# Optimization experiments

Hardware: AMD Instinct MI355X
Metric: run time of the kernel (lower is better)

The kernel has to match this reference:

```python
import jax, jax.numpy as jnp
import numpy as np


def setup_inputs() -> dict:
    key = jax.random.key(0)
    k1, k2 = jax.random.split(key)
    B, C, H, W, S = 8, 128, 256, 256, 1024
    inp = jax.random.normal(k1, (B, C, H, W), dtype=jnp.float32)
    seg = jax.random.randint(k2, (B, H, W), 0, S, dtype=jnp.int32)
    return {"input": inp, "segLabels": seg, "num_segments": S}


def reference(input, segLabels, num_segments):
    # input: [B, C, H, W] float; segLabels: [B, H, W] int in [0, S)
    B, C, H, W = input.shape
    S = num_segments
    N = H * W
    # [B, N, C] pixel features
    feats = jnp.transpose(input.reshape(B, C, N), (0, 2, 1))
    # offset labels so each image's segments occupy a disjoint id range
    ids = (segLabels.reshape(B, N) + jnp.arange(B, dtype=segLabels.dtype)[:, None] * S).reshape(-1)
    flat = feats.reshape(B * N, C)
    sums = jax.ops.segment_sum(flat, ids, num_segments=B * S)          # [B*S, C]
    counts = jax.ops.segment_sum(jnp.ones((B * N,), dtype=input.dtype), ids, num_segments=B * S)  # [B*S]
    avg = sums / jnp.maximum(counts, 1.0)[:, None]
    return avg.reshape(B, S, C)
```

## Files before the change

kernel.cpp:

```cpp
#include <hip/hip_runtime.h>


#define BB 8
#define CC 128
#define NPIX 65536
#define SS 1024
#define TILE 4096
#define NTILES (NPIX / TILE)
#define THREADS 1024

#define POS_ELEMS (BB * NPIX)
#define OFF_ELEMS (BB * NTILES * SS)

__device__ __forceinline__ void lds_barrier() {
  asm volatile("s_waitcnt lgkmcnt(0)\n\ts_barrier" ::: "memory");
}

__global__ __launch_bounds__(THREADS, 1) void sort_kernel(
    const int* __restrict__ seg, unsigned short* __restrict__ pos,
    unsigned short* __restrict__ tileoff) {
  __shared__ unsigned int hist[SS];
  __shared__ unsigned int wsum[16];
  const int b   = blockIdx.x / NTILES;
  const int t   = blockIdx.x % NTILES;
  const int tid = threadIdx.x;

  hist[tid] = 0u;
  __syncthreads();

  const int base = b * NPIX + t * TILE;
  const int4 lab = reinterpret_cast<const int4*>(seg + base)[tid];
  const unsigned int r0 = atomicAdd(&hist[lab.x], 1u);
  const unsigned int r1 = atomicAdd(&hist[lab.y], 1u);
  const unsigned int r2 = atomicAdd(&hist[lab.z], 1u);
  const unsigned int r3 = atomicAdd(&hist[lab.w], 1u);
  __syncthreads();

  const unsigned int cnt = hist[tid];
  unsigned int v = cnt;
  #pragma unroll
  for (int off = 1; off < 64; off <<= 1) {
    const unsigned int u = __shfl_up(v, off);
    if ((tid & 63) >= off) v += u;
  }
  const int w = tid >> 6;
  if ((tid & 63) == 63) wsum[w] = v;
  __syncthreads();
  if (tid < 16) {
    unsigned int x = wsum[tid];
    #pragma unroll
    for (int off = 1; off < 16; off <<= 1) {
      const unsigned int u = __shfl_up(x, off);
      if (tid >= off) x += u;
    }
    wsum[tid] = x;
  }
  __syncthreads();
  const unsigned int woff = (w == 0) ? 0u : wsum[w - 1];
  const unsigned int excl = woff + v - cnt;
  tileoff[(b * NTILES + t) * SS + tid] = (unsigned short)excl;
  hist[tid] = excl;
  __syncthreads();

  ushort4 p4;
  p4.x = (unsigned short)(hist[lab.x] + r0);
  p4.y = (unsigned short)(hist[lab.y] + r1);
  p4.z = (unsigned short)(hist[lab.z] + r2);
  p4.w = (unsigned short)(hist[lab.w] + r3);
  reinterpret_cast<ushort4*>(pos + base)[tid] = p4;
}

__global__ __launch_bounds__(THREADS, 1) void aggr_kernel(
    const float* __restrict__ inp, const unsigned short* __restrict__ pos,
    const unsigned short* __restrict__ tileoff, float* __restrict__ out) {
  __shared__ float4 buf[TILE];
  __shared__ unsigned short offl[SS + 2];

  const int b   = blockIdx.x >> 5;
  const int c0  = (blockIdx.x & 31) << 2;
  const int tid = threadIdx.x;

  const float4* __restrict__ pl0 =
      reinterpret_cast<const float4*>(inp + ((size_t)b * CC + c0) * NPIX);
  const ushort4* __restrict__ pos4 =
      reinterpret_cast<const ushort4*>(pos + (size_t)b * NPIX);
  const int Q = NPIX / 4;

  float a0 = 0.f, a1 = 0.f, a2 = 0.f, a3 = 0.f;
  int cnt = 0;

  float4 cv0 = pl0[tid], cv1 = pl0[tid + Q];
  float4 cv2 = pl0[tid + 2 * Q], cv3 = pl0[tid + 3 * Q];
  ushort4 cp4 = pos4[tid];
  unsigned short coff = tileoff[(b * NTILES + 0) * SS + tid];

  for (int t = 0; t < NTILES; ++t) {
    lds_barrier();
    if (tid == 0) offl[SS] = (unsigned short)TILE;
    offl[tid] = coff;
    buf[cp4.x] = make_float4(cv0.x, cv1.x, cv2.x, cv3.x);
    buf[cp4.y] = make_float4(cv0.y, cv1.y, cv2.y, cv3.y);
    buf[cp4.z] = make_float4(cv0.z, cv1.z, cv2.z, cv3.z);
    buf[cp4.w] = make_float4(cv0.w, cv1.w, cv2.w, cv3.w);

    const int tn = (t + 1 < NTILES) ? t + 1 : t;
    const int pn = tn * (TILE / 4) + tid;
    const float4 nv0 = pl0[pn], nv1 = pl0[pn + Q];
    const float4 nv2 = pl0[pn + 2 * Q], nv3 = pl0[pn + 3 * Q];
    const ushort4 np4 = pos4[pn];
    const unsigned short noff = tileoff[(b * NTILES + tn) * SS + tid];

    lds_barrier();
    const int beg = offl[tid];
    const int end = offl[tid + 1];
    cnt += end - beg;
    for (int j = beg; j < end; ++j) {
      const float4 v = buf[j];
      a0 += v.x; a1 += v.y; a2 += v.z; a3 += v.w;
    }

    cv0 = nv0; cv1 = nv1; cv2 = nv2; cv3 = nv3; cp4 = np4; coff = noff;
  }

  const float inv = 1.0f / (float)max(cnt, 1);
  reinterpret_cast<float4*>(out + ((size_t)(b * SS + tid)) * CC + c0)[0] =
      make_float4(a0 * inv, a1 * inv, a2 * inv, a3 * inv);
}

__global__ __launch_bounds__(THREADS, 1) void seg_avg_kernel(
    const float* __restrict__ inp, const int* __restrict__ seg,
    float* __restrict__ out) {
  __shared__ float acc[SS * 5];
  const int b   = blockIdx.x >> 5;
  const int c0  = (blockIdx.x & 31) << 2;
  const int tid = threadIdx.x;
  for (int i = tid; i < SS * 5; i += THREADS) acc[i] = 0.0f;
  __syncthreads();
  const float4* __restrict__ p0 =
      reinterpret_cast<const float4*>(inp + ((size_t)b * CC + c0) * NPIX);
  const int4* __restrict__ lab = reinterpret_cast<const int4*>(seg + (size_t)b * NPIX);
  const int Q = NPIX / 4;
  int* iacc = reinterpret_cast<int*>(acc);
  for (int i = 0; i < NPIX / (4 * THREADS); ++i) {
    const int p = i * THREADS + tid;
    const int4 s4 = lab[p];
    const float4 v0 = p0[p], v1 = p0[p + Q], v2 = p0[p + 2 * Q], v3 = p0[p + 3 * Q];
    const int a0 = s4.x * 5, a1 = s4.y * 5, a2 = s4.z * 5, a3 = s4.w * 5;
    unsafeAtomicAdd(&acc[a0 + 0], v0.x); unsafeAtomicAdd(&acc[a0 + 1], v1.x);
    unsafeAtomicAdd(&acc[a0 + 2], v2.x); unsafeAtomicAdd(&acc[a0 + 3], v3.x);
    atomicAdd(&iacc[a0 + 4], 1);
    unsafeAtomicAdd(&acc[a1 + 0], v0.y); unsafeAtomicAdd(&acc[a1 + 1], v1.y);
    unsafeAtomicAdd(&acc[a1 + 2], v2.y); unsafeAtomicAdd(&acc[a1 + 3], v3.y);
    atomicAdd(&iacc[a1 + 4], 1);
    unsafeAtomicAdd(&acc[a2 + 0], v0.z); unsafeAtomicAdd(&acc[a2 + 1], v1.z);
    unsafeAtomicAdd(&acc[a2 + 2], v2.z); unsafeAtomicAdd(&acc[a2 + 3], v3.z);
    atomicAdd(&iacc[a2 + 4], 1);
    unsafeAtomicAdd(&acc[a3 + 0], v0.w); unsafeAtomicAdd(&acc[a3 + 1], v1.w);
    unsafeAtomicAdd(&acc[a3 + 2], v2.w); unsafeAtomicAdd(&acc[a3 + 3], v3.w);
    atomicAdd(&iacc[a3 + 4], 1);
  }
  __syncthreads();
  for (int i = tid; i < SS * 4; i += THREADS) {
    const int s = i >> 2, c = i & 3;
    const float cntf = (float)iacc[s * 5 + 4];
    out[((size_t)(b * SS + s)) * CC + c0 + c] = acc[s * 5 + c] / fmaxf(cntf, 1.0f);
  }
}

extern "C" void kernel_launch(void* const* d_in, const int* in_sizes, int n_in,
                              void* d_out, int out_size, void* d_ws, size_t ws_size,
                              hipStream_t stream) {
  const float* inp = (const float*)d_in[0];
  const int*   seg = (const int*)d_in[1];
  float*       out = (float*)d_out;

  const size_t need = (size_t)POS_ELEMS * 2 + (size_t)OFF_ELEMS * 2;
  if (ws_size >= need) {
    unsigned short* pos  = (unsigned short*)d_ws;
    unsigned short* toff = pos + POS_ELEMS;
    sort_kernel<<<BB * NTILES, THREADS, 0, stream>>>(seg, pos, toff);
    aggr_kernel<<<BB * (CC / 4), THREADS, 0, stream>>>(inp, pos, toff, out);
  } else {
    seg_avg_kernel<<<BB * (CC / 4), THREADS, 0, stream>>>(inp, seg, out);
  }
}
```

Baseline: 371.7 us.

## Split aggregation to two channels per block with swizzled LDS and staggered tiles

The aggregation kernel now handles two channels per block instead of four, doubling the grid to 512 blocks and shrinking the LDS buffer to float2 so more blocks can be resident per CU (launch bounds raised to 8). The LDS index is padded with a swizzle to reduce bank conflicts, odd blocks start at a different tile to spread memory traffic, and the gather loop is unrolled by two. The cost is reading the position and offset arrays twice as often, plus full __syncthreads in place of the custom barrier.

```diff
diff --git a/kernel.cpp b/kernel.cpp
--- a/kernel.cpp
+++ b/kernel.cpp
@@ -8,13 +8,12 @@
 #define TILE 4096
 #define NTILES (NPIX / TILE)
 #define THREADS 1024
+#define BUFSZ2 (TILE + TILE / 4)
 
 #define POS_ELEMS (BB * NPIX)
 #define OFF_ELEMS (BB * NTILES * SS)
 
-__device__ __forceinline__ void lds_barrier() {
-  asm volatile("s_waitcnt lgkmcnt(0)\n\ts_barrier" ::: "memory");
-}
+__device__ __forceinline__ int swz2(int e) { return e + (e >> 2); }
 
 __global__ __launch_bounds__(THREADS, 1) void sort_kernel(
     const int* __restrict__ seg, unsigned short* __restrict__ pos,
@@ -70,15 +69,16 @@
   reinterpret_cast<ushort4*>(pos + base)[tid] = p4;
 }
 
-__global__ __launch_bounds__(THREADS, 1) void aggr_kernel(
+__global__ __launch_bounds__(THREADS, 8) void aggr_kernel(
     const float* __restrict__ inp, const unsigned short* __restrict__ pos,
     const unsigned short* __restrict__ tileoff, float* __restrict__ out) {
-  __shared__ float4 buf[TILE];
+  __shared__ float2 buf[BUFSZ2];
   __shared__ unsigned short offl[SS + 2];
 
-  const int b   = blockIdx.x >> 5;
-  const int c0  = (blockIdx.x & 31) << 2;
+  const int b   = blockIdx.x >> 6;
+  const int c0  = (blockIdx.x & 63) << 1;
   const int tid = threadIdx.x;
+  const int tphase = (blockIdx.x & 1) << 3;
 
   const float4* __restrict__ pl0 =
       reinterpret_cast<const float4*>(inp + ((size_t)b * CC + c0) * NPIX);
@@ -86,45 +86,52 @@
       reinterpret_cast<const ushort4*>(pos + (size_t)b * NPIX);
   const int Q = NPIX / 4;
 
-  float a0 = 0.f, a1 = 0.f, a2 = 0.f, a3 = 0.f;
+  float a0 = 0.f, a1 = 0.f;
   int cnt = 0;
 
-  float4 cv0 = pl0[tid], cv1 = pl0[tid + Q];
-  float4 cv2 = pl0[tid + 2 * Q], cv3 = pl0[tid + 3 * Q];
-  ushort4 cp4 = pos4[tid];
-  unsigned short coff = tileoff[(b * NTILES + 0) * SS + tid];
+  int t0 = tphase;
+  int p0i = t0 * (TILE / 4) + tid;
+  float4 cv0 = pl0[p0i], cv1 = pl0[p0i + Q];
+  ushort4 cp4 = pos4[p0i];
+  unsigned short coff = tileoff[(b * NTILES + t0) * SS + tid];
 
-  for (int t = 0; t < NTILES; ++t) {
-    lds_barrier();
+  for (int k = 0; k < NTILES; ++k) {
+    __syncthreads();
     if (tid == 0) offl[SS] = (unsigned short)TILE;
     offl[tid] = coff;
-    buf[cp4.x] = make_float4(cv0.x, cv1.x, cv2.x, cv3.x);
-    buf[cp4.y] = make_float4(cv0.y, cv1.y, cv2.y, cv3.y);
-    buf[cp4.z] = make_float4(cv0.z, cv1.z, cv2.z, cv3.z);
-    buf[cp4.w] = make_float4(cv0.w, cv1.w, cv2.w, cv3.w);
+    buf[swz2(cp4.x)] = make_float2(cv0.x, cv1.x);
+    buf[swz2(cp4.y)] = make_float2(cv0.y, cv1.y);
+    buf[swz2(cp4.z)] = make_float2(cv0.z, cv1.z);
+    buf[swz2(cp4.w)] = make_float2(cv0.w, cv1.w);
 
-    const int tn = (t + 1 < NTILES) ? t + 1 : t;
+    const int kn = (k + 1 < NTILES) ? k + 1 : k;
+    const int tn = (kn + tphase) & (NTILES - 1);
     const int pn = tn * (TILE / 4) + tid;
     const float4 nv0 = pl0[pn], nv1 = pl0[pn + Q];
-    const float4 nv2 = pl0[pn + 2 * Q], nv3 = pl0[pn + 3 * Q];
     const ushort4 np4 = pos4[pn];
     const unsigned short noff = tileoff[(b * NTILES + tn) * SS + tid];
 
-    lds_barrier();
+    __syncthreads();
     const int beg = offl[tid];
     const int end = offl[tid + 1];
     cnt += end - beg;
-    for (int j = beg; j < end; ++j) {
-      const float4 v = buf[j];
-      a0 += v.x; a1 += v.y; a2 += v.z; a3 += v.w;
+    int j = beg;
+    for (; j + 2 <= end; j += 2) {
+      const float2 u = buf[swz2(j)];
+      const float2 v = buf[swz2(j + 1)];
+      a0 += u.x + v.x; a1 += u.y + v.y;
+    }
+    if (j < end) {
+      const float2 u = buf[swz2(j)];
+      a0 += u.x; a1 += u.y;
     }
 
-    cv0 = nv0; cv1 = nv1; cv2 = nv2; cv3 = nv3; cp4 = np4; coff = noff;
+    cv0 = nv0; cv1 = nv1; cp4 = np4; coff = noff;
   }
 
   const float inv = 1.0f / (float)max(cnt, 1);
-  reinterpret_cast<float4*>(out + ((size_t)(b * SS + tid)) * CC + c0)[0] =
-      make_float4(a0 * inv, a1 * inv, a2 * inv, a3 * inv);
+  reinterpret_cast<float2*>(out + ((size_t)(b * SS + tid)) * CC + c0)[0] =
+      make_float2(a0 * inv, a1 * inv);
 }
 
 __global__ __launch_bounds__(THREADS, 1) void seg_avg_kernel(
@@ -179,7 +186,7 @@
     unsigned short* pos  = (unsigned short*)d_ws;
     unsigned short* toff = pos + POS_ELEMS;
     sort_kernel<<<BB * NTILES, THREADS, 0, stream>>>(seg, pos, toff);
-    aggr_kernel<<<BB * (CC / 4), THREADS, 0, stream>>>(inp, pos, toff, out);
+    aggr_kernel<<<BB * (CC / 2), THREADS, 0, stream>>>(inp, pos, toff, out);
   } else {
     seg_avg_kernel<<<BB * (CC / 4), THREADS, 0, stream>>>(inp, seg, out);
   }
```

New measurement: 369.6 us. Within noise of the previous version (-0.6%).
